# Kernel tuning notes

Hardware: AMD Instinct MI355X
Metric: run time of the kernel (lower is better)

The kernel has to match this reference:

```python
import jax, jax.numpy as jnp
import numpy as np

D_MODEL, D_STATE, D_CONV, EXPAND = 1024, 16, 4, 2
D_INNER = EXPAND * D_MODEL          # 2048
DT_RANK = D_MODEL // 16             # 64
B, L = 2, 1024


def setup_inputs() -> dict:
    key = jax.random.key(0)
    ks = jax.random.split(key, 10)
    x = jax.random.normal(ks[0], (B, L, D_MODEL), dtype=jnp.float32)
    ln_w = jnp.ones((D_MODEL,), jnp.float32)
    ln_b = jnp.zeros((D_MODEL,), jnp.float32)
    in_proj_w = jax.random.normal(ks[1], (2 * D_INNER, D_MODEL), jnp.float32) * (D_MODEL ** -0.5)
    conv_w = jax.random.normal(ks[2], (D_INNER, 1, D_CONV), jnp.float32) * (D_CONV ** -0.5)
    conv_b = jnp.zeros((D_INNER,), jnp.float32)
    x_proj_w = jax.random.normal(ks[3], (DT_RANK + 2 * D_STATE, D_INNER), jnp.float32) * (D_INNER ** -0.5)
    dt_proj_w = jax.random.normal(ks[4], (D_INNER, DT_RANK), jnp.float32) * (DT_RANK ** -0.5)
    # dt bias: inverse-softplus of dt sampled log-uniform in [1e-3, 1e-1] (mamba init)
    dt = jnp.exp(jax.random.uniform(ks[5], (D_INNER,)) * (np.log(0.1) - np.log(1e-3)) + np.log(1e-3))
    dt_proj_b = dt + jnp.log(-jnp.expm1(-dt))
    # A_log: log of [1..d_state] repeated per channel (S4D-real init)
    A_log = jnp.log(jnp.broadcast_to(jnp.arange(1, D_STATE + 1, dtype=jnp.float32), (D_INNER, D_STATE)))
    D = jnp.ones((D_INNER,), jnp.float32)
    out_proj_w = jax.random.normal(ks[6], (D_MODEL, D_INNER), jnp.float32) * (D_INNER ** -0.5)
    return dict(x=x, ln_w=ln_w, ln_b=ln_b, in_proj_w=in_proj_w, conv_w=conv_w,
                conv_b=conv_b, x_proj_w=x_proj_w, dt_proj_w=dt_proj_w,
                dt_proj_b=dt_proj_b, A_log=A_log, D=D, out_proj_w=out_proj_w)


def _layernorm(x, w, b, eps=1e-5):
    mu = jnp.mean(x, axis=-1, keepdims=True)
    var = jnp.mean(jnp.square(x - mu), axis=-1, keepdims=True)
    return (x - mu) * jax.lax.rsqrt(var + eps) * w + b


def _mamba(h, in_proj_w, conv_w, conv_b, x_proj_w, dt_proj_w, dt_proj_b, A_log, D, out_proj_w):
    # h: (B, L, d_model)
    xz = jnp.einsum('bld,ed->ble', h, in_proj_w)          # (B,L,2*d_inner)
    x_in, z = jnp.split(xz, 2, axis=-1)                   # each (B,L,d_inner)
    # depthwise causal conv1d
    kernel = jnp.transpose(conv_w, (2, 1, 0))             # (d_conv, 1, d_inner) LIO
    x_conv = jax.lax.conv_general_dilated(
        x_in, kernel, window_strides=(1,), padding=[(D_CONV - 1, 0)],
        dimension_numbers=('NLC', 'LIO', 'NLC'), feature_group_count=D_INNER)
    x_conv = jax.nn.silu(x_conv + conv_b)                 # (B,L,d_inner)
    # input-dependent SSM parameters
    x_dbl = jnp.einsum('bld,ed->ble', x_conv, x_proj_w)   # (B,L,dt_rank+2*d_state)
    dt, B_ssm, C_ssm = jnp.split(x_dbl, [DT_RANK, DT_RANK + D_STATE], axis=-1)
    dt = jax.nn.softplus(jnp.einsum('blr,dr->bld', dt, dt_proj_w) + dt_proj_b)  # (B,L,d_inner)
    A = -jnp.exp(A_log)                                   # (d_inner, d_state)
    deltaA = jnp.exp(dt[..., None] * A)                   # (B,L,d_inner,d_state)
    deltaBu = dt[..., None] * B_ssm[:, :, None, :] * x_conv[..., None]
    # selective scan: h_t = deltaA_t * h_{t-1} + deltaBu_t (parallel associative scan over L)
    def combine(left, right):
        a_l, b_l = left
        a_r, b_r = right
        return a_l * a_r, b_l * a_r + b_r
    _, states = jax.lax.associative_scan(combine, (deltaA, deltaBu), axis=1)
    y = jnp.einsum('blds,bls->bld', states, C_ssm) + x_conv * D
    y = y * jax.nn.silu(z)
    return jnp.einsum('bld,ed->ble', y, out_proj_w)       # (B,L,d_model)


def reference(x, ln_w, ln_b, in_proj_w, conv_w, conv_b, x_proj_w, dt_proj_w,
              dt_proj_b, A_log, D, out_proj_w):
    h = _layernorm(x, ln_w, ln_b)
    return x + _mamba(h, in_proj_w, conv_w, conv_b, x_proj_w, dt_proj_w,
                      dt_proj_b, A_log, D, out_proj_w)
```

## Files before the change

### kernel.cpp

```cpp
#include <hip/hip_runtime.h>
#include <hip/hip_bf16.h>
#include <math.h>

#define DM   1024
#define DI   2048
#define DS   16
#define DTR  64
#define NB   2
#define LL   1024
#define MR   (NB*LL)
#define XDBL 96
#define NC   32
#define CL   32

typedef _Float16 half8  __attribute__((ext_vector_type(8)));
typedef _Float16 half4v __attribute__((ext_vector_type(4)));
typedef float    floatx4 __attribute__((ext_vector_type(4)));

__device__ __forceinline__ void gload_lds16(const void* g, void* l) {
  __builtin_amdgcn_global_load_lds(
      (const __attribute__((address_space(1))) void*)g,
      (__attribute__((address_space(3))) void*)l, 16, 0, 0);
}

__global__ __launch_bounds__(256) void front_kernel(
    const float* __restrict__ x, const float* __restrict__ ln_w,
    const float* __restrict__ ln_b,
    const float* __restrict__ w_in, const float* __restrict__ w_out,
    const float* __restrict__ w_xp, const float* __restrict__ w_dt,
    _Float16* __restrict__ h_h,
    _Float16* __restrict__ w_in_h, _Float16* __restrict__ w_out_h,
    _Float16* __restrict__ w_xp_h, _Float16* __restrict__ w_dt_h) {
  const int blk = blockIdx.x;
  if (blk < MR) {
    __shared__ float sA[4], sB[4];
    const float* xr = x + (size_t)blk * DM;
    float s = 0.f, ss = 0.f;
    for (int i = threadIdx.x; i < DM; i += 256) {
      float v = xr[i];
      s += v; ss += v * v;
    }
    for (int o = 32; o > 0; o >>= 1) {
      s  += __shfl_down(s, o, 64);
      ss += __shfl_down(ss, o, 64);
    }
    const int wid = threadIdx.x >> 6, lid = threadIdx.x & 63;
    if (lid == 0) { sA[wid] = s; sB[wid] = ss; }
    __syncthreads();
    if (threadIdx.x == 0) {
      float S = sA[0] + sA[1] + sA[2] + sA[3];
      float SS = sB[0] + sB[1] + sB[2] + sB[3];
      float mu = S / DM;
      sA[0] = mu;
      sB[0] = rsqrtf(SS / DM - mu * mu + 1e-5f);
    }
    __syncthreads();
    const float mu = sA[0], rs = sB[0];
    for (int i = threadIdx.x; i < DM; i += 256)
      h_h[(size_t)blk * DM + i] = (_Float16)((xr[i] - mu) * rs * ln_w[i] + ln_b[i]);
    return;
  }
  int i = (blk - MR) * 256 + threadIdx.x;
  const int N0 = 1048576, N1 = 524288, N2 = 49152, N3 = 32768;
  const float* s; _Float16* d; int off;
  if (i < N0)            { s = w_in;  d = w_in_h;  off = i; }
  else if (i < N0+N1)    { s = w_out; d = w_out_h; off = i - N0; }
  else if (i < N0+N1+N2) { s = w_xp;  d = w_xp_h;  off = i - N0 - N1; }
  else if (i < N0+N1+N2+N3) { s = w_dt; d = w_dt_h; off = i - N0 - N1 - N2; }
  else return;
  float4 v = ((const float4*)s)[off];
  half4v h = {(_Float16)v.x, (_Float16)v.y, (_Float16)v.z, (_Float16)v.w};
  ((half4v*)d)[off] = h;
}

template <int EPI, int TN>
__global__ __launch_bounds__(256) void gemm_mfma(
    const _Float16* __restrict__ A,
    const _Float16* __restrict__ W,
    void* __restrict__ Cv, void* __restrict__ C2v,
    const float* __restrict__ extra, int ldc,
    int M, int N, int K, int kchunk) {
  constexpr int NT = (TN + 31) / 32;
  constexpr int WSLOT = TN / 16;
  __shared__ alignas(16) _Float16 As[2][128 * 32];
  __shared__ alignas(16) _Float16 Ws[2][TN * 32];
  const int t = threadIdx.x;
  const int wave = t >> 6, lane = t & 63;
  const int m0 = blockIdx.y * 128, n0 = blockIdx.x * TN;
  const int k_beg = blockIdx.z * kchunk;
  const int nk = kchunk >> 5;
  const int wm = (wave >> 1) * 64, wn = (wave & 1) * (TN / 2);
  floatx4 acc[4][NT];
#pragma unroll
  for (int i = 0; i < 4; i++)
#pragma unroll
    for (int j = 0; j < NT; j++) acc[i][j] = {0.f, 0.f, 0.f, 0.f};

  const int fr = lane & 15;
  const int kc8 = lane >> 4;

  auto stage = [&](int buf, int k0) {
    for (int sl = wave; sl < 8; sl += 4) {
      const int idx = sl * 64 + lane;
      const int row = idx >> 2, kc = idx & 3;
      gload_lds16(A + (size_t)(m0 + row) * K + k0 + kc * 8, &As[buf][sl * 512]);
    }
    for (int sl = wave; sl < WSLOT; sl += 4) {
      const int idx = sl * 64 + lane;
      const int row = idx >> 2, kc = idx & 3;
      const int wrow = (n0 + row < N) ? row : 0;
      gload_lds16(W + (size_t)(n0 + wrow) * K + k0 + kc * 8, &Ws[buf][sl * 512]);
    }
  };

  stage(0, k_beg);
  int cur = 0;
  for (int ki = 0; ki < nk; ki++) {
    __syncthreads();
    if (ki + 1 < nk) stage(cur ^ 1, k_beg + ((ki + 1) << 5));
    half8 af[4], wf[NT];
#pragma unroll
    for (int i = 0; i < 4; i++)
      af[i] = *(const half8*)&As[cur][(wm + i * 16 + fr) * 32 + kc8 * 8];
#pragma unroll
    for (int j = 0; j < NT; j++)
      wf[j] = *(const half8*)&Ws[cur][(wn + j * 16 + fr) * 32 + kc8 * 8];
#pragma unroll
    for (int i = 0; i < 4; i++)
#pragma unroll
      for (int j = 0; j < NT; j++)
        acc[i][j] = __builtin_amdgcn_mfma_f32_16x16x32_f16(af[i], wf[j], acc[i][j], 0, 0, 0);
    cur ^= 1;
  }

  const int col = lane & 15, rowq = lane >> 4;
#pragma unroll
  for (int i = 0; i < 4; i++) {
#pragma unroll
    for (int j = 0; j < NT; j++) {
      const int n = n0 + wn + j * 16 + col;
      if (n < N) {
#pragma unroll
        for (int r = 0; r < 4; r++) {
          const int m = m0 + wm + i * 16 + rowq * 4 + r;
          float v = acc[i][j][r];
          if (EPI == 0) {
            if (n < DI) ((_Float16*)Cv )[(size_t)m * DI + n]      = (_Float16)v;
            else        ((_Float16*)C2v)[(size_t)m * DI + n - DI] = (_Float16)v;
          } else if (EPI == 2) {
            ((float*)Cv)[(size_t)m * ldc + n] = v + extra[(size_t)m * ldc + n];
          } else if (EPI == 4) {
            ((float*)Cv)[((size_t)blockIdx.z * M + m) * ldc + n] = v;
          } else if (EPI == 5) {
            v += extra[n];
            v = (v > 20.f) ? v : log1pf(expf(v));
            ((_Float16*)Cv)[(size_t)m * ldc + n] = (_Float16)v;
          }
        }
      }
    }
  }
}

__global__ __launch_bounds__(256) void xproj_reduce(
    const float* __restrict__ part,
    float* __restrict__ x_dbl, _Float16* __restrict__ dtr) {
  const int idx = blockIdx.x * 256 + threadIdx.x;
  const int m = idx / XDBL, c = idx - m * XDBL;
  float s = 0.f;
#pragma unroll
  for (int z = 0; z < 16; z++) s += part[(size_t)z * (MR * XDBL) + idx];
  x_dbl[idx] = s;
  if (c < DTR) dtr[m * DTR + c] = (_Float16)s;
}

__global__ __launch_bounds__(256) void conv_silu_kernel(
    const _Float16* __restrict__ xin, const float* __restrict__ cw,
    const float* __restrict__ cb, _Float16* __restrict__ xc) {
  const int idx = blockIdx.x * 256 + threadIdx.x;
  const int d8 = idx & (DI / 8 - 1);
  const int ml = idx >> 8;
  const int l  = ml & (LL - 1);
  const int d0 = d8 * 8;
  half8 xr[4];
  const half8 zero = {0, 0, 0, 0, 0, 0, 0, 0};
#pragma unroll
  for (int k = 0; k < 4; k++) {
    const int lp = l - 3 + k;
    xr[k] = (lp >= 0) ? *(const half8*)&xin[(size_t)(ml - 3 + k) * DI + d0] : zero;
  }
  half8 o;
#pragma unroll
  for (int j = 0; j < 8; j++) {
    float acc = cb[d0 + j];
#pragma unroll
    for (int k = 0; k < 4; k++)
      acc += (float)xr[k][j] * cw[(d0 + j) * 4 + k];
    o[j] = (_Float16)(acc / (1.f + __expf(-acc)));
  }
  *(half8*)&xc[(size_t)ml * DI + d0] = o;
}

__device__ __forceinline__ bool load_a(const float* __restrict__ A_log, int d,
                                       float* a) {
  const float4* Ap = (const float4*)(A_log + (size_t)d * DS);
  bool fast = true;
#pragma unroll
  for (int i = 0; i < 4; i++) {
    float4 v = Ap[i];
    a[4 * i + 0] = -__expf(v.x); a[4 * i + 1] = -__expf(v.y);
    a[4 * i + 2] = -__expf(v.z); a[4 * i + 3] = -__expf(v.w);
  }
#pragma unroll
  for (int s = 0; s < DS; s++)
    fast = fast && (fabsf(a[s] + (float)(s + 1)) < 1e-4f);
  return fast;
}

__global__ __launch_bounds__(256) void scan_phase1(
    const _Float16* __restrict__ xc,
    const float* __restrict__ xdbl,
    const _Float16* __restrict__ dtm,
    const float* __restrict__ A_log,
    float* __restrict__ HE,
    float* __restrict__ SA) {
  __shared__ float Bs[CL][DS];
  const int bi = blockIdx.x;
  const int dblk = bi & 7;
  const int c = (bi >> 3) & (NC - 1);
  const int b = bi >> 8;
  const int t = threadIdx.x;
  const int d = dblk * 256 + t;
  const int mlbase = b * LL + c * CL;

  for (int i = t; i < CL * DS; i += 256) {
    int tt = i >> 4, s = i & 15;
    Bs[tt][s] = xdbl[(size_t)(mlbase + tt) * XDBL + DTR + s];
  }

  float a[DS];
  const bool fast = load_a(A_log, d, a);
  float h[DS];
#pragma unroll
  for (int s = 0; s < DS; s++) h[s] = 0.f;
  float S = 0.f;
  __syncthreads();

  if (fast) {
    for (int tt = 0; tt < CL; tt++) {
      const size_t ml = mlbase + tt;
      const float dtv = (float)dtm[ml * DI + d];
      const float u   = (float)xc[ml * DI + d];
      const float du  = dtv * u;
      S += dtv;
      const float r = __expf(-dtv);
      float P = 1.f;
#pragma unroll
      for (int s = 0; s < DS; s++) {
        P *= r;
        h[s] = P * h[s] + du * Bs[tt][s];
      }
    }
  } else {
    for (int tt = 0; tt < CL; tt++) {
      const size_t ml = mlbase + tt;
      const float dtv = (float)dtm[ml * DI + d];
      const float u   = (float)xc[ml * DI + d];
      const float du  = dtv * u;
      S += dtv;
#pragma unroll
      for (int s = 0; s < DS; s++)
        h[s] = __expf(dtv * a[s]) * h[s] + du * Bs[tt][s];
    }
  }
  const size_t base = ((size_t)(b * NC + c) * DS) * DI + d;
#pragma unroll
  for (int s = 0; s < DS; s++) HE[base + (size_t)s * DI] = h[s];
  SA[(size_t)(b * NC + c) * DI + d] = S;
}

__global__ __launch_bounds__(256) void scan_phase2(
    const float* __restrict__ A_log,
    const float* __restrict__ SA,
    float* __restrict__ HE) {
  const int idx = blockIdx.x * 256 + threadIdx.x;
  const int d = idx & (DI - 1);
  const int s = (idx >> 11) & (DS - 1);
  const int b = idx >> 15;
  const float a = -__expf(A_log[(size_t)d * DS + s]);
  float Hc = 0.f;
  for (int c = 0; c < NC; c++) {
    const size_t o = ((size_t)(b * NC + c) * DS + s) * DI + d;
    const float he = HE[o];
    const float P = __expf(a * SA[(size_t)(b * NC + c) * DI + d]);
    HE[o] = Hc;
    Hc = P * Hc + he;
  }
}

__global__ __launch_bounds__(256) void scan_phase3(
    const _Float16* __restrict__ xc,
    const float* __restrict__ xdbl,
    const _Float16* __restrict__ dtm,
    const _Float16* __restrict__ zbuf,
    const float* __restrict__ A_log,
    const float* __restrict__ Dvec,
    const float* __restrict__ HE,
    _Float16* __restrict__ y) {
  __shared__ float Bs[CL][DS];
  __shared__ float Cs[CL][DS];
  const int bi = blockIdx.x;
  const int dblk = bi & 7;
  const int c = (bi >> 3) & (NC - 1);
  const int b = bi >> 8;
  const int t = threadIdx.x;
  const int d = dblk * 256 + t;
  const int mlbase = b * LL + c * CL;

  for (int i = t; i < CL * DS; i += 256) {
    int tt = i >> 4, s = i & 15;
    const size_t ro = (size_t)(mlbase + tt) * XDBL + DTR + s;
    Bs[tt][s] = xdbl[ro];
    Cs[tt][s] = xdbl[ro + DS];
  }

  float a[DS];
  const bool fast = load_a(A_log, d, a);
  float h[DS];
  const size_t base = ((size_t)(b * NC + c) * DS) * DI + d;
#pragma unroll
  for (int s = 0; s < DS; s++) h[s] = HE[base + (size_t)s * DI];
  const float Dv = Dvec[d];
  __syncthreads();

  if (fast) {
    for (int tt = 0; tt < CL; tt++) {
      const size_t ml = mlbase + tt;
      const float dtv = (float)dtm[ml * DI + d];
      const float u   = (float)xc[ml * DI + d];
      const float du  = dtv * u;
      const float r = __expf(-dtv);
      float P = 1.f, p = 0.f;
#pragma unroll
      for (int s = 0; s < DS; s++) {
        P *= r;
        h[s] = P * h[s] + du * Bs[tt][s];
        p += h[s] * Cs[tt][s];
      }
      const float zv = (float)zbuf[ml * DI + d];
      const float sil = zv / (1.f + __expf(-zv));
      y[ml * DI + d] = (_Float16)((p + u * Dv) * sil);
    }
  } else {
    for (int tt = 0; tt < CL; tt++) {
      const size_t ml = mlbase + tt;
      const float dtv = (float)dtm[ml * DI + d];
      const float u   = (float)xc[ml * DI + d];
      const float du  = dtv * u;
      float p = 0.f;
#pragma unroll
      for (int s = 0; s < DS; s++) {
        h[s] = __expf(dtv * a[s]) * h[s] + du * Bs[tt][s];
        p += h[s] * Cs[tt][s];
      }
      const float zv = (float)zbuf[ml * DI + d];
      const float sil = zv / (1.f + __expf(-zv));
      y[ml * DI + d] = (_Float16)((p + u * Dv) * sil);
    }
  }
}

extern "C" void kernel_launch(void* const* d_in, const int* in_sizes, int n_in,
                              void* d_out, int out_size, void* d_ws, size_t ws_size,
                              hipStream_t stream) {
  const float* x         = (const float*)d_in[0];
  const float* ln_w      = (const float*)d_in[1];
  const float* ln_b      = (const float*)d_in[2];
  const float* in_proj_w = (const float*)d_in[3];
  const float* conv_w    = (const float*)d_in[4];
  const float* conv_b    = (const float*)d_in[5];
  const float* x_proj_w  = (const float*)d_in[6];
  const float* dt_proj_w = (const float*)d_in[7];
  const float* dt_proj_b = (const float*)d_in[8];
  const float* A_log     = (const float*)d_in[9];
  const float* Dvec      = (const float*)d_in[10];
  const float* out_proj_w= (const float*)d_in[11];
  float* out = (float*)d_out;

  char* ws = (char*)d_ws;
  _Float16* h_h     = (_Float16*)ws;
  _Float16* xin_h   = (_Float16*)(ws + 4194304);
  _Float16* y_h     = xin_h;
  _Float16* z_h     = (_Float16*)(ws + 12582912);
  _Float16* xc_h    = (_Float16*)(ws + 20971520);
  _Float16* dtb_h   = (_Float16*)(ws + 29360128);
  float*    x_dbl   = (float*)   (ws + 46137344);
  float*    SA      = (float*)   (ws + 46923776);
  _Float16* dtr_h   = (_Float16*)(ws + 47448064);
  float*    HE      = (float*)   (ws + 47710208);
  _Float16* w_in_h  = (_Float16*)(ws + 56098816);
  _Float16* w_out_h = (_Float16*)(ws + 64487424);
  _Float16* w_xp_h  = (_Float16*)(ws + 68681728);
  _Float16* w_dt_h  = (_Float16*)(ws + 69074944);
  float*    xp_part = (float*)   (ws + 69337088);

  front_kernel<<<MR + 6464, 256, 0, stream>>>(
      x, ln_w, ln_b, in_proj_w, out_proj_w, x_proj_w, dt_proj_w,
      h_h, w_in_h, w_out_h, w_xp_h, w_dt_h);

  gemm_mfma<0, 32><<<dim3(2 * DI / 32, MR / 128, 1), 256, 0, stream>>>(
      h_h, w_in_h, xin_h, z_h, nullptr, 0, MR, 2 * DI, DM, DM);

  conv_silu_kernel<<<(MR * DI / 8) / 256, 256, 0, stream>>>(xin_h, conv_w, conv_b, xc_h);

  gemm_mfma<4, 96><<<dim3(1, MR / 128, 16), 256, 0, stream>>>(
      xc_h, w_xp_h, xp_part, nullptr, nullptr, XDBL, MR, XDBL, DI, DI / 16);
  xproj_reduce<<<(MR * XDBL) / 256, 256, 0, stream>>>(xp_part, x_dbl, dtr_h);

  gemm_mfma<5, 64><<<dim3(DI / 64, MR / 128, 1), 256, 0, stream>>>(
      dtr_h, w_dt_h, dtb_h, nullptr, dt_proj_b, DI, MR, DI, DTR, DTR);

  scan_phase1<<<NB * NC * (DI / 256), 256, 0, stream>>>(
      xc_h, x_dbl, dtb_h, A_log, HE, SA);
  scan_phase2<<<(NB * DS * DI) / 256, 256, 0, stream>>>(A_log, SA, HE);
  scan_phase3<<<NB * NC * (DI / 256), 256, 0, stream>>>(
      xc_h, x_dbl, dtb_h, z_h, A_log, Dvec, HE, y_h);

  gemm_mfma<2, 32><<<dim3(DM / 32, MR / 128, 1), 256, 0, stream>>>(
      y_h, w_out_h, out, nullptr, x, DM, MR, DM, DI, DI);
}
```

Baseline: 274.4 us.

## Swizzle GEMM LDS layout, enlarge tiles, split-K out_proj with fp16 partials

Applies an XOR swizzle to the LDS k-chunk placement in the MFMA GEMM so fragment reads avoid bank conflicts. The in_proj GEMM moves from 32-wide to 128-wide N tiles for more reuse per block. out_proj becomes a 4-way split-K GEMM writing fp16 partials, followed by a new reduce kernel that also adds the residual, which raises parallelism at the cost of an extra pass. The x_proj partials are also stored in fp16 and softplus uses fast intrinsics, cutting memory traffic but losing some precision.

Result: faster. 227.4 us (-17.1%).

```diff
diff --git a/kernel.cpp b/kernel.cpp
--- a/kernel.cpp
+++ b/kernel.cpp
@@ -98,16 +98,19 @@
 
   const int fr = lane & 15;
   const int kc8 = lane >> 4;
+  const int kp = (kc8 ^ ((fr >> 1) & 3)) * 8;
 
   auto stage = [&](int buf, int k0) {
     for (int sl = wave; sl < 8; sl += 4) {
       const int idx = sl * 64 + lane;
-      const int row = idx >> 2, kc = idx & 3;
+      const int row = idx >> 2;
+      const int kc = (idx & 3) ^ ((row >> 1) & 3);
       gload_lds16(A + (size_t)(m0 + row) * K + k0 + kc * 8, &As[buf][sl * 512]);
     }
     for (int sl = wave; sl < WSLOT; sl += 4) {
       const int idx = sl * 64 + lane;
-      const int row = idx >> 2, kc = idx & 3;
+      const int row = idx >> 2;
+      const int kc = (idx & 3) ^ ((row >> 1) & 3);
       const int wrow = (n0 + row < N) ? row : 0;
       gload_lds16(W + (size_t)(n0 + wrow) * K + k0 + kc * 8, &Ws[buf][sl * 512]);
     }
@@ -121,10 +124,10 @@
     half8 af[4], wf[NT];
 #pragma unroll
     for (int i = 0; i < 4; i++)
-      af[i] = *(const half8*)&As[cur][(wm + i * 16 + fr) * 32 + kc8 * 8];
+      af[i] = *(const half8*)&As[cur][(wm + i * 16 + fr) * 32 + kp];
 #pragma unroll
     for (int j = 0; j < NT; j++)
-      wf[j] = *(const half8*)&Ws[cur][(wn + j * 16 + fr) * 32 + kc8 * 8];
+      wf[j] = *(const half8*)&Ws[cur][(wn + j * 16 + fr) * 32 + kp];
 #pragma unroll
     for (int i = 0; i < 4; i++)
 #pragma unroll
@@ -147,13 +150,11 @@
           if (EPI == 0) {
             if (n < DI) ((_Float16*)Cv )[(size_t)m * DI + n]      = (_Float16)v;
             else        ((_Float16*)C2v)[(size_t)m * DI + n - DI] = (_Float16)v;
-          } else if (EPI == 2) {
-            ((float*)Cv)[(size_t)m * ldc + n] = v + extra[(size_t)m * ldc + n];
           } else if (EPI == 4) {
-            ((float*)Cv)[((size_t)blockIdx.z * M + m) * ldc + n] = v;
+            ((_Float16*)Cv)[((size_t)blockIdx.z * M + m) * ldc + n] = (_Float16)v;
           } else if (EPI == 5) {
             v += extra[n];
-            v = (v > 20.f) ? v : log1pf(expf(v));
+            v = (v > 20.f) ? v : __logf(1.f + __expf(v));
             ((_Float16*)Cv)[(size_t)m * ldc + n] = (_Float16)v;
           }
         }
@@ -163,15 +164,28 @@
 }
 
 __global__ __launch_bounds__(256) void xproj_reduce(
-    const float* __restrict__ part,
+    const _Float16* __restrict__ part,
     float* __restrict__ x_dbl, _Float16* __restrict__ dtr) {
   const int idx = blockIdx.x * 256 + threadIdx.x;
   const int m = idx / XDBL, c = idx - m * XDBL;
   float s = 0.f;
 #pragma unroll
-  for (int z = 0; z < 16; z++) s += part[(size_t)z * (MR * XDBL) + idx];
+  for (int z = 0; z < 16; z++) s += (float)part[(size_t)z * (MR * XDBL) + idx];
   x_dbl[idx] = s;
   if (c < DTR) dtr[m * DTR + c] = (_Float16)s;
+}
+
+__global__ __launch_bounds__(256) void out_reduce(
+    const float* __restrict__ x, const _Float16* __restrict__ part,
+    float* __restrict__ out) {
+  const int i = blockIdx.x * 256 + threadIdx.x;
+  float4 a = ((const float4*)x)[i];
+#pragma unroll
+  for (int z = 0; z < 4; z++) {
+    half4v p = ((const half4v*)(part + (size_t)z * MR * DM))[i];
+    a.x += (float)p.x; a.y += (float)p.y; a.z += (float)p.z; a.w += (float)p.w;
+  }
+  ((float4*)out)[i] = a;
 }
 
 __global__ __launch_bounds__(256) void conv_silu_kernel(
@@ -388,27 +402,28 @@
   float* out = (float*)d_out;
 
   char* ws = (char*)d_ws;
-  _Float16* h_h     = (_Float16*)ws;
-  _Float16* xin_h   = (_Float16*)(ws + 4194304);
-  _Float16* y_h     = xin_h;
-  _Float16* z_h     = (_Float16*)(ws + 12582912);
-  _Float16* xc_h    = (_Float16*)(ws + 20971520);
-  _Float16* dtb_h   = (_Float16*)(ws + 29360128);
-  float*    x_dbl   = (float*)   (ws + 46137344);
-  float*    SA      = (float*)   (ws + 46923776);
-  _Float16* dtr_h   = (_Float16*)(ws + 47448064);
-  float*    HE      = (float*)   (ws + 47710208);
-  _Float16* w_in_h  = (_Float16*)(ws + 56098816);
-  _Float16* w_out_h = (_Float16*)(ws + 64487424);
-  _Float16* w_xp_h  = (_Float16*)(ws + 68681728);
-  _Float16* w_dt_h  = (_Float16*)(ws + 69074944);
-  float*    xp_part = (float*)   (ws + 69337088);
+  _Float16* h_h      = (_Float16*)ws;
+  _Float16* xin_h    = (_Float16*)(ws + 4194304);
+  _Float16* y_h      = xin_h;
+  _Float16* z_h      = (_Float16*)(ws + 12582912);
+  _Float16* xc_h     = (_Float16*)(ws + 20971520);
+  _Float16* dtb_h    = (_Float16*)(ws + 29360128);
+  _Float16* out_part = dtb_h;
+  float*    x_dbl    = (float*)   (ws + 46137344);
+  float*    SA       = (float*)   (ws + 46923776);
+  _Float16* dtr_h    = (_Float16*)(ws + 47448064);
+  float*    HE       = (float*)   (ws + 47710208);
+  _Float16* w_in_h   = (_Float16*)(ws + 56098816);
+  _Float16* w_out_h  = (_Float16*)(ws + 64487424);
+  _Float16* w_xp_h   = (_Float16*)(ws + 68681728);
+  _Float16* w_dt_h   = (_Float16*)(ws + 69074944);
+  _Float16* xp_part  = (_Float16*)(ws + 69337088);
 
   front_kernel<<<MR + 6464, 256, 0, stream>>>(
       x, ln_w, ln_b, in_proj_w, out_proj_w, x_proj_w, dt_proj_w,
       h_h, w_in_h, w_out_h, w_xp_h, w_dt_h);
 
-  gemm_mfma<0, 32><<<dim3(2 * DI / 32, MR / 128, 1), 256, 0, stream>>>(
+  gemm_mfma<0, 128><<<dim3(2 * DI / 128, MR / 128, 1), 256, 0, stream>>>(
       h_h, w_in_h, xin_h, z_h, nullptr, 0, MR, 2 * DI, DM, DM);
 
   conv_silu_kernel<<<(MR * DI / 8) / 256, 256, 0, stream>>>(xin_h, conv_w, conv_b, xc_h);
@@ -426,6 +441,7 @@
   scan_phase3<<<NB * NC * (DI / 256), 256, 0, stream>>>(
       xc_h, x_dbl, dtb_h, z_h, A_log, Dvec, HE, y_h);
 
-  gemm_mfma<2, 32><<<dim3(DM / 32, MR / 128, 1), 256, 0, stream>>>(
-      y_h, w_out_h, out, nullptr, x, DM, MR, DM, DI, DI);
-}
+  gemm_mfma<4, 128><<<dim3(DM / 128, MR / 128, 4), 256, 0, stream>>>(
+      y_h, w_out_h, out_part, nullptr, nullptr, DM, MR, DM, DI, DI / 4);
+  out_reduce<<<(MR * DM / 4) / 256, 256, 0, stream>>>(x, out_part, out);
+}
```
